# Performance work log

Hardware: AMD Instinct MI355X
Metric: run time of the kernel (lower is better)

The kernel has to match this reference:

```python
import jax, jax.numpy as jnp
import numpy as np

B, S, H, V, T = 32, 128, 256, 32000, 100


def setup_inputs() -> dict:
    key = jax.random.key(0)
    ks = jax.random.split(key, 16)
    s = 1.0 / np.sqrt(H)

    def u(k, shape):
        return jax.random.uniform(k, shape, jnp.float32, -s, s)

    return dict(
        enc_outputs=jax.random.normal(ks[0], (B, S, H), jnp.float32),
        enc_hidden=jax.random.normal(ks[1], (1, B, H), jnp.float32),
        target_tensor=jax.random.randint(ks[2], (B, T), 0, V),
        embedding=u(ks[3], (V, H)),
        Qw=u(ks[4], (H, H)), Qb=u(ks[5], (H,)),
        Kw=u(ks[6], (H, H)), Kb=u(ks[7], (H,)),
        Vw=u(ks[8], (1, H)), Vb=u(ks[9], (1,)),
        W_ih=u(ks[10], (3 * H, 2 * H)), W_hh=u(ks[11], (3 * H, H)),
        b_ih=u(ks[12], (3 * H,)), b_hh=u(ks[13], (3 * H,)),
        out_w=u(ks[14], (V, H)), out_b=u(ks[15], (V,)),
    )


def reference(enc_outputs, enc_hidden, target_tensor, embedding,
              Qw, Qb, Kw, Kb, Vw, Vb, W_ih, W_hh, b_ih, b_hh, out_w, out_b):
    # Teacher-forcing decode: dec_input starts at token 0, then target[:, i].
    Bv, Sv, Hd = enc_outputs.shape
    Tv = target_tensor.shape[1]
    # K(keys) is step-invariant: precompute once (same math as in-loop Linear).
    enc_k = enc_outputs @ Kw.T + Kb  # (B,S,H)
    tokens = jnp.concatenate(
        [jnp.zeros((Bv, 1), target_tensor.dtype), target_tensor[:, :-1]], axis=1)
    tokens_t = tokens.T  # (T,B)

    def step(h, tok):
        emb = embedding[tok]                                  # (B,H), dropout=eval noop
        q = h @ Qw.T + Qb                                     # query from hidden
        e = jnp.tanh(q[:, None, :] + enc_k)                   # (B,S,H) additive attn
        scores = jnp.einsum('bsh,h->bs', e, Vw[0]) + Vb[0]    # (B,S)
        w = jax.nn.softmax(scores, axis=-1)
        ctx = jnp.einsum('bs,bsh->bh', w, enc_outputs)        # bmm(weights, keys)
        x = jnp.concatenate([emb, ctx], axis=-1)              # (B,2H)
        gi = x @ W_ih.T + b_ih
        gh = h @ W_hh.T + b_hh
        r = jax.nn.sigmoid(gi[:, :Hd] + gh[:, :Hd])
        z = jax.nn.sigmoid(gi[:, Hd:2 * Hd] + gh[:, Hd:2 * Hd])
        n = jnp.tanh(gi[:, 2 * Hd:] + r * gh[:, 2 * Hd:])
        h_new = (1.0 - z) * n + z * h                         # torch GRU cell
        logits = h_new @ out_w.T + out_b                      # (B,V)
        return h_new, (logits, w)

    h_final, (logits, atts) = jax.lax.scan(step, enc_hidden[0], tokens_t)
    dec_outputs = jax.nn.log_softmax(jnp.transpose(logits, (1, 0, 2)), axis=-1)  # (B,T,V)
    atts = jnp.transpose(atts, (1, 0, 2))                     # (B,T,S)
    return dec_outputs, h_final[None], atts
```

## Files before the change

### kernel.cpp

```cpp
#include <hip/hip_runtime.h>
#include <hip/hip_bf16.h>

#define Bn 32
#define Sn 128
#define Hn 256
#define Vn 32000
#define Tn 100
#define GIn 768
#define AGENT __HIP_MEMORY_SCOPE_AGENT

typedef __attribute__((ext_vector_type(8))) short bf16x8;
typedef __attribute__((ext_vector_type(4))) float f32x4;

__device__ __forceinline__ float frcp(float x){ return __builtin_amdgcn_rcpf(x); }
__device__ __forceinline__ float ftanh(float x){ return 1.0f - 2.0f*frcp(__expf(2.0f*x)+1.0f); }
__device__ __forceinline__ float fsigm(float x){ return frcp(1.0f + __expf(-x)); }
__device__ __forceinline__ float b2f(unsigned short u){
  unsigned int v = ((unsigned int)u) << 16; return __builtin_bit_cast(float, v);
}
__device__ __forceinline__ unsigned short f2bu(float f){
  unsigned int u = __builtin_bit_cast(unsigned int, f);
  u += 0x7FFFu + ((u >> 16) & 1u);
  return (unsigned short)(u >> 16);
}
__device__ __forceinline__ void st_ag(float* p, float v){
  __hip_atomic_store(p, v, __ATOMIC_RELAXED, AGENT);
}
__device__ __forceinline__ float ld_ag(float* p){
  return __hip_atomic_load(p, __ATOMIC_RELAXED, AGENT);
}

__global__ __launch_bounds__(256) void k_tr(const float* __restrict__ in,
    float* __restrict__ out, int R, int C)
{
  __shared__ float tile[32][33];
  const int bx = blockIdx.x*32, by = blockIdx.y*32;
  const int tx = threadIdx.x & 31, ty = threadIdx.x >> 5;
  #pragma unroll
  for(int r = ty; r < 32; r += 8)
    if(by + r < R && bx + tx < C) tile[r][tx] = in[(size_t)(by + r)*C + bx + tx];
  __syncthreads();
  #pragma unroll
  for(int r = ty; r < 32; r += 8)
    if(bx + r < C && by + tx < R) out[(size_t)(bx + r)*R + by + tx] = tile[tx][r];
}

__global__ __launch_bounds__(256) void k_packW1R(const float* __restrict__ Qw,
    const float* __restrict__ Whh, unsigned short* __restrict__ W1R)
{
  const int tid = blockIdx.x*256 + threadIdx.x;
  const int lane = tid & 63;
  const int fragid = tid >> 6;
  const int frag = fragid & 31, w = (fragid >> 5) & 7, hb = fragid >> 8;
  const int kk = frag >> 2, tt = frag & 3;
  const int lr = lane & 15, lg = lane >> 4;
  const int base = (hb == 0) ? (w < 4 ? 0 : 768) : (w < 4 ? 256 : 512);
  const int f = base + (w & 3)*64 + tt*16 + lr;
  const int col = kk*32 + lg*8;
  const float* src = (f < 256 ? Qw + (size_t)f*Hn : Whh + (size_t)(f - 256)*Hn) + col;
  float4 v0 = *(const float4*)src, v1 = *(const float4*)(src + 4);
  unsigned short* d = W1R + ((size_t)fragid*64 + lane)*8;
  d[0]=f2bu(v0.x); d[1]=f2bu(v0.y); d[2]=f2bu(v0.z); d[3]=f2bu(v0.w);
  d[4]=f2bu(v1.x); d[5]=f2bu(v1.y); d[6]=f2bu(v1.z); d[7]=f2bu(v1.w);
}

__global__ __launch_bounds__(256) void k_cvt(const float* __restrict__ src,
    __hip_bfloat16* __restrict__ dst, int n)
{
  int i = (blockIdx.x*256 + threadIdx.x)*4;
  if(i < n){
    float4 v = *(const float4*)(src + i);
    dst[i+0] = __float2bfloat16(v.x);
    dst[i+1] = __float2bfloat16(v.y);
    dst[i+2] = __float2bfloat16(v.z);
    dst[i+3] = __float2bfloat16(v.w);
  }
}

__global__ __launch_bounds__(256) void k_enc2(const float* __restrict__ enc_outputs,
    const float* __restrict__ KwT, const float* __restrict__ Kb,
    unsigned short* __restrict__ enc_kb16)
{
  const int r0 = blockIdx.x*16, j = threadIdx.x;
  __shared__ __align__(16) float encl[Hn][20];
  #pragma unroll
  for(int r = 0; r < 16; r++) encl[j][r] = enc_outputs[(size_t)(r0 + r)*Hn + j];
  __syncthreads();
  float acc[16];
  #pragma unroll
  for(int r = 0; r < 16; r++) acc[r] = Kb[j];
  for(int d = 0; d < Hn; d++){
    const float wv = KwT[(size_t)d*Hn + j];
    const float4 e0 = *(const float4*)&encl[d][0];
    const float4 e1 = *(const float4*)&encl[d][4];
    const float4 e2 = *(const float4*)&encl[d][8];
    const float4 e3 = *(const float4*)&encl[d][12];
    acc[0]+=e0.x*wv; acc[1]+=e0.y*wv; acc[2]+=e0.z*wv; acc[3]+=e0.w*wv;
    acc[4]+=e1.x*wv; acc[5]+=e1.y*wv; acc[6]+=e1.z*wv; acc[7]+=e1.w*wv;
    acc[8]+=e2.x*wv; acc[9]+=e2.y*wv; acc[10]+=e2.z*wv; acc[11]+=e2.w*wv;
    acc[12]+=e3.x*wv; acc[13]+=e3.y*wv; acc[14]+=e3.z*wv; acc[15]+=e3.w*wv;
  }
  #pragma unroll
  for(int r = 0; r < 16; r++) enc_kb16[(size_t)(r0 + r)*Hn + j] = f2bu(acc[r]);
}

__global__ __launch_bounds__(256) void k_packEk(const unsigned short* __restrict__ enc_kb16,
    unsigned short* __restrict__ ekP)
{
  const int tid = blockIdx.x*256 + threadIdx.x;
  const int b = tid >> 12;
  const int o = tid & 4095;
  const int g = o >> 6, l = o & 63;
  const int w = g >> 3, i = g & 7;
  const int s = w*16 + (l >> 2);
  const int e0 = i*32 + (l & 3)*8;
  const int4 v = *(const int4*)(enc_kb16 + ((size_t)(b*Sn + s))*Hn + e0);
  *(int4*)(ekP + (size_t)b*32768 + (size_t)o*8) = v;
}

__global__ __launch_bounds__(768) void k_encW2b(const float* __restrict__ enc_outputs,
    const float* __restrict__ W_ihT, unsigned short* __restrict__ encW2P)
{
  const int r0 = blockIdx.x*16, tid = threadIdx.x;
  __shared__ __align__(16) float encl[Hn][20];
  if(tid < Hn){
    #pragma unroll
    for(int r = 0; r < 16; r++) encl[tid][r] = enc_outputs[(size_t)(r0 + r)*Hn + tid];
  }
  __syncthreads();
  float acc[16];
  #pragma unroll
  for(int r = 0; r < 16; r++) acc[r] = 0.f;
  for(int d = 0; d < Hn; d++){
    const float wv = W_ihT[(size_t)(Hn + d)*GIn + tid];
    const float4 e0 = *(const float4*)&encl[d][0];
    const float4 e1 = *(const float4*)&encl[d][4];
    const float4 e2 = *(const float4*)&encl[d][8];
    const float4 e3 = *(const float4*)&encl[d][12];
    acc[0]+=e0.x*wv; acc[1]+=e0.y*wv; acc[2]+=e0.z*wv; acc[3]+=e0.w*wv;
    acc[4]+=e1.x*wv; acc[5]+=e1.y*wv; acc[6]+=e1.z*wv; acc[7]+=e1.w*wv;
    acc[8]+=e2.x*wv; acc[9]+=e2.y*wv; acc[10]+=e2.z*wv; acc[11]+=e2.w*wv;
    acc[12]+=e3.x*wv; acc[13]+=e3.y*wv; acc[14]+=e3.z*wv; acc[15]+=e3.w*wv;
  }
  const int hb = (tid >= 384) ? 1 : 0;
  const int c = tid - hb*384;
  #pragma unroll
  for(int r = 0; r < 16; r++){
    const int bs = r0 + r;
    const int bb = bs >> 7, ss = bs & 127;
    encW2P[(((size_t)bb*2 + hb)*384 + c)*128 + ss] = f2bu(acc[r]);
  }
}

__global__ __launch_bounds__(768) void k_giemb2(const int* __restrict__ target,
    const float* __restrict__ embedding, const float* __restrict__ W_ihT,
    const float* __restrict__ b_ih, float* __restrict__ gi_emb)
{
  const int r0 = blockIdx.x*16, tid = threadIdx.x;
  __shared__ __align__(16) float embl[Hn][20];
  if(tid < Hn){
    #pragma unroll
    for(int r = 0; r < 16; r++){
      const int row = r0 + r;
      const int t = row >> 5, b = row & 31;
      const int tok = (t == 0) ? 0 : target[b*Tn + (t-1)];
      embl[tid][r] = embedding[(size_t)tok*Hn + tid];
    }
  }
  __syncthreads();
  float acc[16];
  #pragma unroll
  for(int r = 0; r < 16; r++) acc[r] = b_ih[tid];
  for(int d = 0; d < Hn; d++){
    const float wv = W_ihT[(size_t)d*GIn + tid];
    const float4 e0 = *(const float4*)&embl[d][0];
    const float4 e1 = *(const float4*)&embl[d][4];
    const float4 e2 = *(const float4*)&embl[d][8];
    const float4 e3 = *(const float4*)&embl[d][12];
    acc[0]+=e0.x*wv; acc[1]+=e0.y*wv; acc[2]+=e0.z*wv; acc[3]+=e0.w*wv;
    acc[4]+=e1.x*wv; acc[5]+=e1.y*wv; acc[6]+=e1.z*wv; acc[7]+=e1.w*wv;
    acc[8]+=e2.x*wv; acc[9]+=e2.y*wv; acc[10]+=e2.z*wv; acc[11]+=e2.w*wv;
    acc[12]+=e3.x*wv; acc[13]+=e3.y*wv; acc[14]+=e3.z*wv; acc[15]+=e3.w*wv;
  }
  #pragma unroll
  for(int r = 0; r < 16; r++) gi_emb[(size_t)(r0 + r)*GIn + tid] = acc[r];
}

__global__ __launch_bounds__(512, 2) void k_loop4(
    const float* __restrict__ enc_hidden,
    const unsigned short* __restrict__ ekP,
    const unsigned short* __restrict__ encW2P,
    const unsigned short* __restrict__ W1R,
    const float* __restrict__ Qb, const float* __restrict__ b_hh,
    const float* __restrict__ Vw, const float* __restrict__ Vb,
    const float* __restrict__ gi_emb,
    __hip_bfloat16* __restrict__ h_all,
    float* __restrict__ atts_out,
    float* __restrict__ hfin_out,
    float* qbuf,
    float* gbuf,
    unsigned int* qflag,
    unsigned int* gflag)
{
  const int p = (blockIdx.x & 7)*4 + (blockIdx.x >> 4);
  const int half = (blockIdx.x >> 3) & 1;
  const int b = p;
  const int tid = threadIdx.x;
  const int lane = tid & 63, wv = tid >> 6;
  const int lg = lane >> 4;

  __shared__ __align__(16) unsigned short ek_l[32768];
  __shared__ __align__(16) unsigned short ew_l[256*136];
  __shared__ __align__(16) float h_sh[Hn];
  __shared__ __align__(16) short h_b16[Hn];
  __shared__ __align__(16) float qgh_sh[1024];
  __shared__ __align__(16) float vw_sh[Hn];
  __shared__ __align__(16) float sc_sh[Sn];
  __shared__ __align__(16) float w_sh[Sn];
  __shared__ __align__(16) float gic_sh[GIn];

  {
    const unsigned short* src = ekP + (size_t)b*32768;
    #pragma unroll
    for(int c = 0; c < 8; c++){
      const int idx = (c*512 + tid)*8;
      *(int4*)(ek_l + idx) = *(const int4*)(src + idx);
    }
  }
  {
    const unsigned short* src = encW2P + ((size_t)(b*2 + half)*384)*128;
    #pragma unroll
    for(int i = 0; i < 8; i++){
      const int id = i*512 + tid;
      const int c = id >> 4, sc = id & 15;
      *(int4*)(ew_l + c*136 + sc*8) = *(const int4*)(src + (size_t)c*128 + sc*8);
    }
  }
  bf16x8 er0, er1, er2, er3;
  {
    const unsigned short* esrc = encW2P +
        ((size_t)((b*2 + half)*384 + 256 + (tid >> 2)))*128 + (tid & 3)*32;
    er0 = *(const bf16x8*)(esrc);
    er1 = *(const bf16x8*)(esrc + 8);
    er2 = *(const bf16x8*)(esrc + 16);
    er3 = *(const bf16x8*)(esrc + 24);
  }
  bf16x8 w1f[32];
  {
    const unsigned short* wsrc = W1R + (((size_t)(half*8 + wv)*32)*64 + lane)*8;
    #pragma unroll
    for(int f = 0; f < 32; f++) w1f[f] = *(const bf16x8*)(wsrc + (size_t)f*512);
  }
  const int fbase = (half == 0) ? (wv < 4 ? 0 : 768) : (wv < 4 ? 256 : 512);
  float bias_r[4];
  #pragma unroll
  for(int tt = 0; tt < 4; tt++){
    const int f = fbase + (wv & 3)*64 + tt*16 + (lane & 15);
    bias_r[tt] = (f < Hn) ? Qb[f] : b_hh[f - Hn];
  }
  if(tid < Hn){
    float hv = enc_hidden[b*Hn + tid];
    h_sh[tid] = hv; h_b16[tid] = (short)f2bu(hv);
    vw_sh[tid] = Vw[tid];
  }
  __syncthreads();
  const float vb0 = Vb[0];
  const int s2 = tid >> 2, g2 = tid & 3;

  for(int t = 0; t < Tn; t++){
    const int par = t & 1;
    {
      f32x4 acc[4];
      #pragma unroll
      for(int tt = 0; tt < 4; tt++) acc[tt] = (f32x4){0.f,0.f,0.f,0.f};
      #pragma unroll
      for(int kk = 0; kk < 8; kk++){
        bf16x8 a = *(const bf16x8*)(h_b16 + kk*32 + lg*8);
        #pragma unroll
        for(int tt = 0; tt < 4; tt++)
          acc[tt] = __builtin_amdgcn_mfma_f32_16x16x32_bf16(a, w1f[kk*4 + tt], acc[tt], 0, 0, 0);
      }
      if(lane < 16){
        #pragma unroll
        for(int tt = 0; tt < 4; tt++){
          const float v = acc[tt][0] + bias_r[tt];
          qgh_sh[fbase + (wv & 3)*64 + tt*16 + lane] = v;
          st_ag(&qbuf[((size_t)(par*32 + p)*2 + half)*512 + wv*64 + tt*16 + lane], v);
        }
      }
    }
    __syncthreads();
    if(tid == 0){
      __threadfence();
      __hip_atomic_store(&qflag[p*2 + half], (unsigned)(t + 1), __ATOMIC_RELEASE, AGENT);
      long cnt = 0;
      while(__hip_atomic_load(&qflag[p*2 + (half^1)], __ATOMIC_ACQUIRE, AGENT) < (unsigned)(t + 1)
            && ++cnt < 10000000L){}
    }
    __syncthreads();
    {
      const int pw = tid >> 6, rem = tid & 63;
      const int pbase = ((half^1) == 0) ? (pw < 4 ? 0 : 768) : (pw < 4 ? 256 : 512);
      const float v = ld_ag(&qbuf[((size_t)(par*32 + p)*2 + (half^1))*512 + tid]);
      qgh_sh[pbase + (pw & 3)*64 + rem] = v;
    }
    __syncthreads();

    {
      float pacc = 0.f;
      #pragma unroll
      for(int i = 0; i < 8; i++){
        bf16x8 e8 = *(const bf16x8*)(ek_l + ((wv*8 + i) << 9) + lane*8);
        const int kb = i*32 + g2*8;
        #pragma unroll
        for(int j = 0; j < 8; j++){
          float ev = b2f((unsigned short)e8[j]);
          pacc = fmaf(vw_sh[kb + j], ftanh(qgh_sh[kb + j] + ev), pacc);
        }
      }
      pacc += __shfl_xor(pacc, 1); pacc += __shfl_xor(pacc, 2);
      if(g2 == 0) sc_sh[s2] = pacc + vb0;
    }
    __syncthreads();

    if(tid < 64){
      float v0 = sc_sh[tid], v1 = sc_sh[tid + 64];
      float m = fmaxf(v0, v1);
      #pragma unroll
      for(int off = 1; off < 64; off <<= 1) m = fmaxf(m, __shfl_xor(m, off));
      float e0 = __expf(v0 - m), e1 = __expf(v1 - m);
      float sm = e0 + e1;
      #pragma unroll
      for(int off = 1; off < 64; off <<= 1) sm += __shfl_xor(sm, off);
      float inv = frcp(sm);
      float w0 = e0*inv, w1 = e1*inv;
      w_sh[tid] = w0; w_sh[tid + 64] = w1;
      if(half == 0){
        float* ao = atts_out + ((size_t)b*Tn + t)*Sn;
        ao[tid] = w0; ao[tid + 64] = w1;
      }
    }
    __syncthreads();

    float ge0 = 0.f, ge1 = 0.f, ge2 = 0.f;
    if(tid < Hn){
      const float* ge = gi_emb + ((size_t)t*Bn + b)*GIn;
      ge0 = ge[tid]; ge1 = ge[Hn + tid]; ge2 = ge[2*Hn + tid];
    }

    {
      const int c3 = tid >> 1, s3 = (tid & 1)*64;
      float a3 = 0.f;
      #pragma unroll
      for(int i = 0; i < 8; i++){
        bf16x8 e = *(const bf16x8*)(ew_l + c3*136 + s3 + i*8);
        const float4 wa = *(const float4*)&w_sh[s3 + i*8];
        const float4 wb = *(const float4*)&w_sh[s3 + i*8 + 4];
        a3 = fmaf(wa.x, b2f((unsigned short)e[0]), a3);
        a3 = fmaf(wa.y, b2f((unsigned short)e[1]), a3);
        a3 = fmaf(wa.z, b2f((unsigned short)e[2]), a3);
        a3 = fmaf(wa.w, b2f((unsigned short)e[3]), a3);
        a3 = fmaf(wb.x, b2f((unsigned short)e[4]), a3);
        a3 = fmaf(wb.y, b2f((unsigned short)e[5]), a3);
        a3 = fmaf(wb.z, b2f((unsigned short)e[6]), a3);
        a3 = fmaf(wb.w, b2f((unsigned short)e[7]), a3);
      }
      a3 += __shfl_xor(a3, 1);
      if((tid & 1) == 0){
        gic_sh[half*384 + c3] = a3;
        st_ag(&gbuf[((size_t)(par*32 + p)*2 + half)*384 + c3], a3);
      }
      const float* wq = &w_sh[(tid & 3)*32];
      float r2 = 0.f;
      #pragma unroll
      for(int j = 0; j < 8; j++) r2 = fmaf(wq[j],      b2f((unsigned short)er0[j]), r2);
      #pragma unroll
      for(int j = 0; j < 8; j++) r2 = fmaf(wq[8 + j],  b2f((unsigned short)er1[j]), r2);
      #pragma unroll
      for(int j = 0; j < 8; j++) r2 = fmaf(wq[16 + j], b2f((unsigned short)er2[j]), r2);
      #pragma unroll
      for(int j = 0; j < 8; j++) r2 = fmaf(wq[24 + j], b2f((unsigned short)er3[j]), r2);
      r2 += __shfl_xor(r2, 1); r2 += __shfl_xor(r2, 2);
      if((tid & 3) == 0){
        const int c = 256 + (tid >> 2);
        gic_sh[half*384 + c] = r2;
        st_ag(&gbuf[((size_t)(par*32 + p)*2 + half)*384 + c], r2);
      }
    }
    __syncthreads();
    if(tid == 0){
      __threadfence();
      __hip_atomic_store(&gflag[p*2 + half], (unsigned)(t + 1), __ATOMIC_RELEASE, AGENT);
      long cnt = 0;
      while(__hip_atomic_load(&gflag[p*2 + (half^1)], __ATOMIC_ACQUIRE, AGENT) < (unsigned)(t + 1)
            && ++cnt < 10000000L){}
    }
    __syncthreads();
    if(tid < 384)
      gic_sh[(half^1)*384 + tid] = ld_ag(&gbuf[((size_t)(par*32 + p)*2 + (half^1))*384 + tid]);
    __syncthreads();

    if(tid < Hn){
      float gr = ge0 + gic_sh[tid];
      float gz = ge1 + gic_sh[Hn + tid];
      float gn = ge2 + gic_sh[2*Hn + tid];
      float r = fsigm(gr + qgh_sh[256 + tid]);
      float z = fsigm(gz + qgh_sh[512 + tid]);
      float n = ftanh(gn + r*qgh_sh[768 + tid]);
      float hn2 = (1.0f - z)*n + z*h_sh[tid];
      if(half == 0){
        h_all[((size_t)t*Bn + b)*Hn + tid] = __float2bfloat16(hn2);
        if(t == Tn-1) hfin_out[b*Hn + tid] = hn2;
      }
      h_sh[tid] = hn2;
      h_b16[tid] = (short)f2bu(hn2);
    }
    __syncthreads();
  }
}

__global__ __launch_bounds__(512, 2) void k_logits2(
    const short* __restrict__ h_all, const short* __restrict__ w_bf,
    const float* __restrict__ out_b,
    float* __restrict__ pmax, float* __restrict__ psum,
    const float* __restrict__ lse, float* __restrict__ dec_out,
    int pass)
{
  const int tid = threadIdx.x;
  const int wave = tid >> 6, lane = tid & 63;
  const int lr = lane & 15, lg = lane >> 4;
  const int wm = wave >> 2, wn = wave & 3;
  const int n0 = blockIdx.x*256 + wn*64;
  const int m0 = blockIdx.y*256 + wm*128;
  f32x4 acc[8][4];
  #pragma unroll
  for(int mt = 0; mt < 8; mt++)
    #pragma unroll
    for(int nt = 0; nt < 4; nt++) acc[mt][nt] = (f32x4){0.f,0.f,0.f,0.f};
  #pragma unroll
  for(int kk = 0; kk < 8; kk++){
    bf16x8 am[8], bn[4];
    #pragma unroll
    for(int mt = 0; mt < 8; mt++){
      int row = m0 + mt*16 + lr; row = row < 3200 ? row : 3199;
      am[mt] = *(const bf16x8*)(h_all + (size_t)row*Hn + kk*32 + lg*8);
    }
    #pragma unroll
    for(int nt = 0; nt < 4; nt++)
      bn[nt] = *(const bf16x8*)(w_bf + (size_t)(n0 + nt*16 + lr)*Hn + kk*32 + lg*8);
    #pragma unroll
    for(int mt = 0; mt < 8; mt++)
      #pragma unroll
      for(int nt = 0; nt < 4; nt++)
        acc[mt][nt] = __builtin_amdgcn_mfma_f32_16x16x32_bf16(am[mt], bn[nt], acc[mt][nt], 0, 0, 0);
  }
  float bias[4];
  #pragma unroll
  for(int nt = 0; nt < 4; nt++) bias[nt] = out_b[n0 + nt*16 + lr];

  if(pass == 0){
    __shared__ float pm_l[256][4];
    __shared__ float ps_l[256][4];
    #pragma unroll
    for(int mt = 0; mt < 8; mt++){
      #pragma unroll
      for(int i = 0; i < 4; i++){
        float v0 = acc[mt][0][i] + bias[0], v1 = acc[mt][1][i] + bias[1];
        float v2 = acc[mt][2][i] + bias[2], v3 = acc[mt][3][i] + bias[3];
        float m = fmaxf(fmaxf(v0, v1), fmaxf(v2, v3));
        m = fmaxf(m, __shfl_xor(m, 1)); m = fmaxf(m, __shfl_xor(m, 2));
        m = fmaxf(m, __shfl_xor(m, 4)); m = fmaxf(m, __shfl_xor(m, 8));
        float s = __expf(v0 - m) + __expf(v1 - m) + __expf(v2 - m) + __expf(v3 - m);
        s += __shfl_xor(s, 1); s += __shfl_xor(s, 2);
        s += __shfl_xor(s, 4); s += __shfl_xor(s, 8);
        if(lr == 0){
          const int rl = wm*128 + mt*16 + lg*4 + i;
          pm_l[rl][wn] = m; ps_l[rl][wn] = s;
        }
      }
    }
    __syncthreads();
    if(tid < 256){
      const int rg = blockIdx.y*256 + tid;
      if(rg < 3200){
        float m = fmaxf(fmaxf(pm_l[tid][0], pm_l[tid][1]), fmaxf(pm_l[tid][2], pm_l[tid][3]));
        float s = ps_l[tid][0]*__expf(pm_l[tid][0] - m) + ps_l[tid][1]*__expf(pm_l[tid][1] - m)
                + ps_l[tid][2]*__expf(pm_l[tid][2] - m) + ps_l[tid][3]*__expf(pm_l[tid][3] - m);
        pmax[(size_t)blockIdx.x*3200 + rg] = m;
        psum[(size_t)blockIdx.x*3200 + rg] = s;
      }
    }
  } else {
    #pragma unroll
    for(int mt = 0; mt < 8; mt++){
      #pragma unroll
      for(int i = 0; i < 4; i++){
        const int rg = blockIdx.y*256 + wm*128 + mt*16 + lg*4 + i;
        if(rg < 3200){
          const float l = lse[rg];
          const int bb = rg & 31, tt2 = rg >> 5;
          float* dst = dec_out + (size_t)bb*((size_t)Tn*Vn) + (size_t)tt2*Vn + n0;
          dst[ 0 + lr] = acc[mt][0][i] + bias[0] - l;
          dst[16 + lr] = acc[mt][1][i] + bias[1] - l;
          dst[32 + lr] = acc[mt][2][i] + bias[2] - l;
          dst[48 + lr] = acc[mt][3][i] + bias[3] - l;
        }
      }
    }
  }
}

__global__ __launch_bounds__(256) void k_lse(const float* __restrict__ pmax,
    const float* __restrict__ psum, float* __restrict__ lse)
{
  const int row = blockIdx.x*256 + threadIdx.x;
  if(row >= Tn*Bn) return;
  float m = -3.0e38f;
  for(int c = 0; c < 125; c++) m = fmaxf(m, pmax[(size_t)c*3200 + row]);
  float s = 0.f;
  for(int c = 0; c < 125; c++)
    s += psum[(size_t)c*3200 + row] * __expf(pmax[(size_t)c*3200 + row] - m);
  lse[row] = m + __logf(s);
}

extern "C" void kernel_launch(void* const* d_in, const int* in_sizes, int n_in,
                              void* d_out, int out_size, void* d_ws, size_t ws_size,
                              hipStream_t stream)
{
  const float* enc_outputs = (const float*)d_in[0];
  const float* enc_hidden  = (const float*)d_in[1];
  const int*   target      = (const int*)d_in[2];
  const float* embedding   = (const float*)d_in[3];
  const float* Qw   = (const float*)d_in[4];
  const float* Qb   = (const float*)d_in[5];
  const float* Kw   = (const float*)d_in[6];
  const float* Kb   = (const float*)d_in[7];
  const float* Vw   = (const float*)d_in[8];
  const float* Vb   = (const float*)d_in[9];
  const float* W_ih = (const float*)d_in[10];
  const float* W_hh = (const float*)d_in[11];
  const float* b_ih = (const float*)d_in[12];
  const float* b_hh = (const float*)d_in[13];
  const float* out_w = (const float*)d_in[14];
  const float* out_b = (const float*)d_in[15];

  float* dec  = (float*)d_out;
  float* hfin = dec + (size_t)Bn*Tn*Vn;
  float* atts = hfin + Bn*Hn;

  unsigned short* enc_kb16 = (unsigned short*)(dec);
  unsigned short* ekP      = (unsigned short*)(dec + 524288);
  unsigned short* encW2P   = (unsigned short*)(dec + 1048576);
  float* gi_emb = dec + 2621440;
  float* W_ihT  = dec + 5079040;
  float* KwT    = dec + 5472256;
  float* pmax   = dec + 5537792;
  float* psum   = dec + 5937792;
  unsigned short* W1R = (unsigned short*)(dec + 6337792);
  float* qbuf   = dec + 6468864;
  float* gbuf   = dec + 6534400;
  unsigned int* qflag = (unsigned int*)(dec + 6583552);
  unsigned int* gflag = qflag + 64;

  float* wsf = (float*)d_ws;
  float* lse = wsf;
  __hip_bfloat16* h_all = (__hip_bfloat16*)(wsf + 3200);
  __hip_bfloat16* w_bf  = h_all + (size_t)Tn*Bn*Hn;

  k_tr     <<<dim3(8, 8),   dim3(256), 0, stream>>>(Kw, KwT, 256, 256);
  k_tr     <<<dim3(16, 24), dim3(256), 0, stream>>>(W_ih, W_ihT, 768, 512);
  k_packW1R<<<dim3(128),    dim3(256), 0, stream>>>(Qw, W_hh, W1R);
  k_cvt    <<<dim3((Vn*Hn)/1024), dim3(256), 0, stream>>>(out_w, w_bf, Vn*Hn);
  k_enc2   <<<dim3(256), dim3(256), 0, stream>>>(enc_outputs, KwT, Kb, enc_kb16);
  k_packEk <<<dim3(512), dim3(256), 0, stream>>>(enc_kb16, ekP);
  k_encW2b <<<dim3(256), dim3(768), 0, stream>>>(enc_outputs, W_ihT, encW2P);
  k_giemb2 <<<dim3(200), dim3(768), 0, stream>>>(target, embedding, W_ihT, b_ih, gi_emb);

  hipMemsetAsync((void*)qflag, 0, 128*sizeof(unsigned int), stream);

  k_loop4 <<<dim3(64), dim3(512), 0, stream>>>(enc_hidden, ekP, encW2P, W1R,
            Qb, b_hh, Vw, Vb, gi_emb, h_all, atts, hfin,
            qbuf, gbuf, qflag, gflag);

  k_logits2<<<dim3(125, 13), dim3(512), 0, stream>>>(
            (const short*)h_all, (const short*)w_bf, out_b,
            pmax, psum, (const float*)nullptr, (float*)nullptr, 0);
  k_lse    <<<dim3(13), dim3(256), 0, stream>>>(pmax, psum, lse);
  k_logits2<<<dim3(125, 13), dim3(512), 0, stream>>>(
            (const short*)h_all, (const short*)w_bf, out_b,
            (float*)nullptr, (float*)nullptr, lse, dec, 1);
}
```

Baseline: 1.467 ms.

## Split GRU hidden state across block pair, exchange only new h once per step

Reorganises the two-block-per-batch recurrent loop. Each block now redundantly computes the full query projection plus its own half of the W_hh gates, and owns half of the hidden units. Blocks exchange only the packed bf16 halves of the new hidden state, which replaces two cross-block flag handshakes (query and context gates) with one per step. The context-weight LDS tile also switches from padded rows to an XOR swizzle. The trade is more MFMA work and register-held weight fragments (40 instead of 32) per block, in exchange for fewer inter-block barriers on the serial critical path.

```diff
diff --git a/kernel.cpp b/kernel.cpp
--- a/kernel.cpp
+++ b/kernel.cpp
@@ -23,10 +23,10 @@
   u += 0x7FFFu + ((u >> 16) & 1u);
   return (unsigned short)(u >> 16);
 }
-__device__ __forceinline__ void st_ag(float* p, float v){
+__device__ __forceinline__ void st_ag_u(unsigned int* p, unsigned int v){
   __hip_atomic_store(p, v, __ATOMIC_RELAXED, AGENT);
 }
-__device__ __forceinline__ float ld_ag(float* p){
+__device__ __forceinline__ unsigned int ld_ag_u(unsigned int* p){
   return __hip_atomic_load(p, __ATOMIC_RELAXED, AGENT);
 }
 
@@ -51,14 +51,22 @@
   const int tid = blockIdx.x*256 + threadIdx.x;
   const int lane = tid & 63;
   const int fragid = tid >> 6;
-  const int frag = fragid & 31, w = (fragid >> 5) & 7, hb = fragid >> 8;
-  const int kk = frag >> 2, tt = frag & 3;
+  const int tt = fragid % 5;
+  const int kk = (fragid/5) % 8;
+  const int w  = (fragid/40) % 8;
+  const int hb = fragid/320;
   const int lr = lane & 15, lg = lane >> 4;
-  const int base = (hb == 0) ? (w < 4 ? 0 : 768) : (w < 4 ? 256 : 512);
-  const int f = base + (w & 3)*64 + tt*16 + lr;
+  const float* src;
+  if(tt < 2){
+    const int f = w*32 + tt*16 + lr;
+    src = Qw + (size_t)f*Hn;
+  } else {
+    const int lf = w*48 + (tt-2)*16 + lr;
+    const int g = lf >> 7, jj = lf & 127;
+    src = Whh + (size_t)(g*256 + hb*128 + jj)*Hn;
+  }
   const int col = kk*32 + lg*8;
-  const float* src = (f < 256 ? Qw + (size_t)f*Hn : Whh + (size_t)(f - 256)*Hn) + col;
-  float4 v0 = *(const float4*)src, v1 = *(const float4*)(src + 4);
+  float4 v0 = *(const float4*)(src + col), v1 = *(const float4*)(src + col + 4);
   unsigned short* d = W1R + ((size_t)fragid*64 + lane)*8;
   d[0]=f2bu(v0.x); d[1]=f2bu(v0.y); d[2]=f2bu(v0.z); d[3]=f2bu(v0.w);
   d[4]=f2bu(v1.x); d[5]=f2bu(v1.y); d[6]=f2bu(v1.z); d[7]=f2bu(v1.w);
@@ -142,8 +150,8 @@
     acc[8]+=e2.x*wv; acc[9]+=e2.y*wv; acc[10]+=e2.z*wv; acc[11]+=e2.w*wv;
     acc[12]+=e3.x*wv; acc[13]+=e3.y*wv; acc[14]+=e3.z*wv; acc[15]+=e3.w*wv;
   }
-  const int hb = (tid >= 384) ? 1 : 0;
-  const int c = tid - hb*384;
+  const int g = tid >> 8, jj = tid & 255;
+  const int hb = jj >> 7, c = g*128 + (jj & 127);
   #pragma unroll
   for(int r = 0; r < 16; r++){
     const int bs = r0 + r;
@@ -186,7 +194,7 @@
   for(int r = 0; r < 16; r++) gi_emb[(size_t)(r0 + r)*GIn + tid] = acc[r];
 }
 
-__global__ __launch_bounds__(512, 2) void k_loop4(
+__global__ __launch_bounds__(512, 2) void k_loop5(
     const float* __restrict__ enc_hidden,
     const unsigned short* __restrict__ ekP,
     const unsigned short* __restrict__ encW2P,
@@ -197,27 +205,23 @@
     __hip_bfloat16* __restrict__ h_all,
     float* __restrict__ atts_out,
     float* __restrict__ hfin_out,
-    float* qbuf,
-    float* gbuf,
-    unsigned int* qflag,
-    unsigned int* gflag)
-{
-  const int p = (blockIdx.x & 7)*4 + (blockIdx.x >> 4);
-  const int half = (blockIdx.x >> 3) & 1;
-  const int b = p;
+    unsigned int* hbuf,
+    unsigned int* hflag)
+{
+  const int p = blockIdx.x >> 1, hb = blockIdx.x & 1, b = p;
   const int tid = threadIdx.x;
   const int lane = tid & 63, wv = tid >> 6;
-  const int lg = lane >> 4;
+  const int lr = lane & 15, lg = lane >> 4;
 
   __shared__ __align__(16) unsigned short ek_l[32768];
-  __shared__ __align__(16) unsigned short ew_l[256*136];
-  __shared__ __align__(16) float h_sh[Hn];
+  __shared__ __align__(16) unsigned short ew_l[32768];
+  __shared__ __align__(16) float h_sh[128];
   __shared__ __align__(16) short h_b16[Hn];
   __shared__ __align__(16) float qgh_sh[1024];
   __shared__ __align__(16) float vw_sh[Hn];
   __shared__ __align__(16) float sc_sh[Sn];
   __shared__ __align__(16) float w_sh[Sn];
-  __shared__ __align__(16) float gic_sh[GIn];
+  __shared__ __align__(16) float gic_l[384];
 
   {
     const unsigned short* src = ekP + (size_t)b*32768;
@@ -228,41 +232,49 @@
     }
   }
   {
-    const unsigned short* src = encW2P + ((size_t)(b*2 + half)*384)*128;
+    const unsigned short* src = encW2P + ((size_t)(b*2 + hb)*384)*128;
     #pragma unroll
     for(int i = 0; i < 8; i++){
       const int id = i*512 + tid;
-      const int c = id >> 4, sc = id & 15;
-      *(int4*)(ew_l + c*136 + sc*8) = *(const int4*)(src + (size_t)c*128 + sc*8);
+      const int c = id >> 4, sg = id & 15;
+      *(int4*)(ew_l + c*128 + ((sg ^ (c & 15)) << 3)) =
+          *(const int4*)(src + (size_t)c*128 + sg*8);
     }
   }
   bf16x8 er0, er1, er2, er3;
   {
     const unsigned short* esrc = encW2P +
-        ((size_t)((b*2 + half)*384 + 256 + (tid >> 2)))*128 + (tid & 3)*32;
+        ((size_t)((b*2 + hb)*384 + 256 + (tid >> 2)))*128 + (tid & 3)*32;
     er0 = *(const bf16x8*)(esrc);
     er1 = *(const bf16x8*)(esrc + 8);
     er2 = *(const bf16x8*)(esrc + 16);
     er3 = *(const bf16x8*)(esrc + 24);
   }
-  bf16x8 w1f[32];
+  bf16x8 w1f[40];
   {
-    const unsigned short* wsrc = W1R + (((size_t)(half*8 + wv)*32)*64 + lane)*8;
-    #pragma unroll
-    for(int f = 0; f < 32; f++) w1f[f] = *(const bf16x8*)(wsrc + (size_t)f*512);
-  }
-  const int fbase = (half == 0) ? (wv < 4 ? 0 : 768) : (wv < 4 ? 256 : 512);
-  float bias_r[4];
-  #pragma unroll
-  for(int tt = 0; tt < 4; tt++){
-    const int f = fbase + (wv & 3)*64 + tt*16 + (lane & 15);
-    bias_r[tt] = (f < Hn) ? Qb[f] : b_hh[f - Hn];
+    const unsigned short* wsrc = W1R + (((size_t)(hb*8 + wv)*40)*64 + lane)*8;
+    #pragma unroll
+    for(int f = 0; f < 40; f++) w1f[f] = *(const bf16x8*)(wsrc + (size_t)f*512);
+  }
+  float bias_r[5]; int idx_r[5];
+  #pragma unroll
+  for(int tt = 0; tt < 2; tt++){
+    const int f = wv*32 + tt*16 + lr;
+    bias_r[tt] = Qb[f]; idx_r[tt] = f;
+  }
+  #pragma unroll
+  for(int tt = 2; tt < 5; tt++){
+    const int lf = wv*48 + (tt-2)*16 + lr;
+    const int g = lf >> 7, jj = lf & 127;
+    bias_r[tt] = b_hh[g*256 + hb*128 + jj];
+    idx_r[tt]  = 256 + g*256 + hb*128 + jj;
   }
   if(tid < Hn){
     float hv = enc_hidden[b*Hn + tid];
-    h_sh[tid] = hv; h_b16[tid] = (short)f2bu(hv);
+    h_b16[tid] = (short)f2bu(hv);
     vw_sh[tid] = Vw[tid];
   }
+  if(tid < 128) h_sh[tid] = enc_hidden[b*Hn + hb*128 + tid];
   __syncthreads();
   const float vb0 = Vb[0];
   const int s2 = tid >> 2, g2 = tid & 3;
@@ -270,39 +282,21 @@
   for(int t = 0; t < Tn; t++){
     const int par = t & 1;
     {
-      f32x4 acc[4];
-      #pragma unroll
-      for(int tt = 0; tt < 4; tt++) acc[tt] = (f32x4){0.f,0.f,0.f,0.f};
+      f32x4 acc[5];
+      #pragma unroll
+      for(int tt = 0; tt < 5; tt++) acc[tt] = (f32x4){0.f,0.f,0.f,0.f};
       #pragma unroll
       for(int kk = 0; kk < 8; kk++){
         bf16x8 a = *(const bf16x8*)(h_b16 + kk*32 + lg*8);
         #pragma unroll
-        for(int tt = 0; tt < 4; tt++)
-          acc[tt] = __builtin_amdgcn_mfma_f32_16x16x32_bf16(a, w1f[kk*4 + tt], acc[tt], 0, 0, 0);
+        for(int tt = 0; tt < 5; tt++)
+          acc[tt] = __builtin_amdgcn_mfma_f32_16x16x32_bf16(a, w1f[kk*5 + tt], acc[tt], 0, 0, 0);
       }
       if(lane < 16){
         #pragma unroll
-        for(int tt = 0; tt < 4; tt++){
-          const float v = acc[tt][0] + bias_r[tt];
-          qgh_sh[fbase + (wv & 3)*64 + tt*16 + lane] = v;
-          st_ag(&qbuf[((size_t)(par*32 + p)*2 + half)*512 + wv*64 + tt*16 + lane], v);
-        }
-      }
-    }
-    __syncthreads();
-    if(tid == 0){
-      __threadfence();
-      __hip_atomic_store(&qflag[p*2 + half], (unsigned)(t + 1), __ATOMIC_RELEASE, AGENT);
-      long cnt = 0;
-      while(__hip_atomic_load(&qflag[p*2 + (half^1)], __ATOMIC_ACQUIRE, AGENT) < (unsigned)(t + 1)
-            && ++cnt < 10000000L){}
-    }
-    __syncthreads();
-    {
-      const int pw = tid >> 6, rem = tid & 63;
-      const int pbase = ((half^1) == 0) ? (pw < 4 ? 0 : 768) : (pw < 4 ? 256 : 512);
-      const float v = ld_ag(&qbuf[((size_t)(par*32 + p)*2 + (half^1))*512 + tid]);
-      qgh_sh[pbase + (pw & 3)*64 + rem] = v;
+        for(int tt = 0; tt < 5; tt++)
+          qgh_sh[idx_r[tt]] = acc[tt][0] + bias_r[tt];
+      }
     }
     __syncthreads();
 
@@ -335,7 +329,7 @@
       float inv = frcp(sm);
       float w0 = e0*inv, w1 = e1*inv;
       w_sh[tid] = w0; w_sh[tid + 64] = w1;
-      if(half == 0){
+      if(hb == 0){
         float* ao = atts_out + ((size_t)b*Tn + t)*Sn;
         ao[tid] = w0; ao[tid + 64] = w1;
       }
@@ -343,19 +337,19 @@
     __syncthreads();
 
     float ge0 = 0.f, ge1 = 0.f, ge2 = 0.f;
-    if(tid < Hn){
-      const float* ge = gi_emb + ((size_t)t*Bn + b)*GIn;
-      ge0 = ge[tid]; ge1 = ge[Hn + tid]; ge2 = ge[2*Hn + tid];
+    if(tid < 128){
+      const float* ge = gi_emb + ((size_t)t*Bn + b)*GIn + hb*128 + tid;
+      ge0 = ge[0]; ge1 = ge[256]; ge2 = ge[512];
     }
 
     {
-      const int c3 = tid >> 1, s3 = (tid & 1)*64;
+      const int c3 = tid >> 1, s3 = tid & 1;
       float a3 = 0.f;
       #pragma unroll
       for(int i = 0; i < 8; i++){
-        bf16x8 e = *(const bf16x8*)(ew_l + c3*136 + s3 + i*8);
-        const float4 wa = *(const float4*)&w_sh[s3 + i*8];
-        const float4 wb = *(const float4*)&w_sh[s3 + i*8 + 4];
+        bf16x8 e = *(const bf16x8*)(ew_l + c3*128 + ((((s3 << 3) + i) ^ (c3 & 15)) << 3));
+        const float4 wa = *(const float4*)&w_sh[s3*64 + i*8];
+        const float4 wb = *(const float4*)&w_sh[s3*64 + i*8 + 4];
         a3 = fmaf(wa.x, b2f((unsigned short)e[0]), a3);
         a3 = fmaf(wa.y, b2f((unsigned short)e[1]), a3);
         a3 = fmaf(wa.z, b2f((unsigned short)e[2]), a3);
@@ -366,10 +360,7 @@
         a3 = fmaf(wb.w, b2f((unsigned short)e[7]), a3);
       }
       a3 += __shfl_xor(a3, 1);
-      if((tid & 1) == 0){
-        gic_sh[half*384 + c3] = a3;
-        st_ag(&gbuf[((size_t)(par*32 + p)*2 + half)*384 + c3], a3);
-      }
+      if(!(tid & 1)) gic_l[c3] = a3;
       const float* wq = &w_sh[(tid & 3)*32];
       float r2 = 0.f;
       #pragma unroll
@@ -381,41 +372,48 @@
       #pragma unroll
       for(int j = 0; j < 8; j++) r2 = fmaf(wq[24 + j], b2f((unsigned short)er3[j]), r2);
       r2 += __shfl_xor(r2, 1); r2 += __shfl_xor(r2, 2);
-      if((tid & 3) == 0){
-        const int c = 256 + (tid >> 2);
-        gic_sh[half*384 + c] = r2;
-        st_ag(&gbuf[((size_t)(par*32 + p)*2 + half)*384 + c], r2);
-      }
+      if(!(tid & 3)) gic_l[256 + (tid >> 2)] = r2;
     }
     __syncthreads();
-    if(tid == 0){
-      __threadfence();
-      __hip_atomic_store(&gflag[p*2 + half], (unsigned)(t + 1), __ATOMIC_RELEASE, AGENT);
-      long cnt = 0;
-      while(__hip_atomic_load(&gflag[p*2 + (half^1)], __ATOMIC_ACQUIRE, AGENT) < (unsigned)(t + 1)
-            && ++cnt < 10000000L){}
+
+    if(tid < 128){
+      float gr = ge0 + gic_l[tid];
+      float gz = ge1 + gic_l[128 + tid];
+      float gn = ge2 + gic_l[256 + tid];
+      const int jg = hb*128 + tid;
+      float r = fsigm(gr + qgh_sh[256 + jg]);
+      float z = fsigm(gz + qgh_sh[512 + jg]);
+      float n = ftanh(gn + r*qgh_sh[768 + jg]);
+      float hn2 = (1.0f - z)*n + z*h_sh[tid];
+      h_sh[tid] = hn2;
+      const unsigned short hb16 = f2bu(hn2);
+      h_b16[jg] = (short)hb16;
+      h_all[((size_t)t*Bn + b)*Hn + jg] = __float2bfloat16(hn2);
+      if(t == Tn-1) hfin_out[b*Hn + jg] = hn2;
+      if(t < Tn-1){
+        float hnx = __shfl_down(hn2, 1);
+        if(!(tid & 1)){
+          unsigned int u = (unsigned int)hb16 | ((unsigned int)f2bu(hnx) << 16);
+          st_ag_u(&hbuf[((size_t)(par*32 + p)*2 + hb)*64 + (tid >> 1)], u);
+        }
+      }
     }
     __syncthreads();
-    if(tid < 384)
-      gic_sh[(half^1)*384 + tid] = ld_ag(&gbuf[((size_t)(par*32 + p)*2 + (half^1))*384 + tid]);
-    __syncthreads();
-
-    if(tid < Hn){
-      float gr = ge0 + gic_sh[tid];
-      float gz = ge1 + gic_sh[Hn + tid];
-      float gn = ge2 + gic_sh[2*Hn + tid];
-      float r = fsigm(gr + qgh_sh[256 + tid]);
-      float z = fsigm(gz + qgh_sh[512 + tid]);
-      float n = ftanh(gn + r*qgh_sh[768 + tid]);
-      float hn2 = (1.0f - z)*n + z*h_sh[tid];
-      if(half == 0){
-        h_all[((size_t)t*Bn + b)*Hn + tid] = __float2bfloat16(hn2);
-        if(t == Tn-1) hfin_out[b*Hn + tid] = hn2;
-      }
-      h_sh[tid] = hn2;
-      h_b16[tid] = (short)f2bu(hn2);
-    }
-    __syncthreads();
+
+    if(t < Tn-1){
+      if(tid == 0){
+        __hip_atomic_store(&hflag[p*2 + hb], (unsigned)(t + 1), __ATOMIC_RELEASE, AGENT);
+        long cnt = 0;
+        while(__hip_atomic_load(&hflag[p*2 + (hb^1)], __ATOMIC_ACQUIRE, AGENT) < (unsigned)(t + 1)
+              && ++cnt < 10000000L){}
+      }
+      __syncthreads();
+      if(tid < 64){
+        unsigned int u = ld_ag_u(&hbuf[((size_t)(par*32 + p)*2 + (hb^1))*64 + tid]);
+        ((unsigned int*)h_b16)[(hb^1)*64 + tid] = u;
+      }
+      __syncthreads();
+    }
   }
 }
 
@@ -557,10 +555,8 @@
   float* pmax   = dec + 5537792;
   float* psum   = dec + 5937792;
   unsigned short* W1R = (unsigned short*)(dec + 6337792);
-  float* qbuf   = dec + 6468864;
-  float* gbuf   = dec + 6534400;
-  unsigned int* qflag = (unsigned int*)(dec + 6583552);
-  unsigned int* gflag = qflag + 64;
+  unsigned int* hbuf  = (unsigned int*)(dec + 6501632);
+  unsigned int* hflag = (unsigned int*)(dec + 6509824);
 
   float* wsf = (float*)d_ws;
   float* lse = wsf;
@@ -569,18 +565,17 @@
 
   k_tr     <<<dim3(8, 8),   dim3(256), 0, stream>>>(Kw, KwT, 256, 256);
   k_tr     <<<dim3(16, 24), dim3(256), 0, stream>>>(W_ih, W_ihT, 768, 512);
-  k_packW1R<<<dim3(128),    dim3(256), 0, stream>>>(Qw, W_hh, W1R);
+  k_packW1R<<<dim3(160),    dim3(256), 0, stream>>>(Qw, W_hh, W1R);
   k_cvt    <<<dim3((Vn*Hn)/1024), dim3(256), 0, stream>>>(out_w, w_bf, Vn*Hn);
   k_enc2   <<<dim3(256), dim3(256), 0, stream>>>(enc_outputs, KwT, Kb, enc_kb16);
   k_packEk <<<dim3(512), dim3(256), 0, stream>>>(enc_kb16, ekP);
   k_encW2b <<<dim3(256), dim3(768), 0, stream>>>(enc_outputs, W_ihT, encW2P);
   k_giemb2 <<<dim3(200), dim3(768), 0, stream>>>(target, embedding, W_ihT, b_ih, gi_emb);
 
-  hipMemsetAsync((void*)qflag, 0, 128*sizeof(unsigned int), stream);
-
-  k_loop4 <<<dim3(64), dim3(512), 0, stream>>>(enc_hidden, ekP, encW2P, W1R,
-            Qb, b_hh, Vw, Vb, gi_emb, h_all, atts, hfin,
-            qbuf, gbuf, qflag, gflag);
+  hipMemsetAsync((void*)hflag, 0, 64*sizeof(unsigned int), stream);
+
+  k_loop5 <<<dim3(64), dim3(512), 0, stream>>>(enc_hidden, ekP, encW2P, W1R,
+            Qb, b_hh, Vw, Vb, gi_emb, h_all, atts, hfin, hbuf, hflag);
 
   k_logits2<<<dim3(125, 13), dim3(512), 0, stream>>>(
             (const short*)h_all, (const short*)w_bf, out_b,
```

Result: faster. 1.373 ms (-6.4%).
